# Optimization experiments

Hardware: AMD Instinct MI355X
Metric: run time of the kernel (lower is better)

The kernel has to match this reference:

```python
import jax, jax.numpy as jnp
import numpy as np
from jax import lax

INP_MODES = (4, 8, 8, 4)
OUT_MODES = (4, 8, 8, 4)
RANKS = (1, 8, 8, 8, 1)  # mat_ranks
WINDOW = (3, 3)


def setup_inputs() -> dict:
    key = jax.random.key(0)
    ks = jax.random.split(key, 7)
    d = {}
    d["x"] = jax.random.normal(ks[0], (16, 32, 32, 1024), jnp.float32)
    # conv filter: [kh, kw, 1, r0]
    d["filters"] = jax.random.normal(ks[1], (WINDOW[0], WINDOW[1], 1, RANKS[0]), jnp.float32) * (1.0 / 3.0)
    # TT cores: core_i has shape [m_i * r_{i+1}, r_i * n_i]
    for i in range(4):
        shp = (OUT_MODES[i] * RANKS[i + 1], RANKS[i] * INP_MODES[i])
        d[f"core{i}"] = jax.random.normal(ks[2 + i], shp, jnp.float32) * (1.0 / np.sqrt(shp[1]).astype(np.float32))
    d["bias"] = jnp.zeros((int(np.prod(OUT_MODES)),), jnp.float32)
    return d


def tt_conv(x, filters, cores, bias):
    B, H, W, C = x.shape  # C == prod(INP_MODES)
    r0 = filters.shape[3]
    # depthwise-style: every channel of every batch item becomes its own 1-channel map
    tmp = x.transpose(0, 3, 1, 2).reshape(B * C, H, W, 1)
    tmp = lax.conv_general_dilated(tmp, filters, window_strides=(1, 1), padding="SAME",
                                   dimension_numbers=("NHWC", "HWIO", "NHWC"))
    h, w = tmp.shape[1], tmp.shape[2]
    # [B, C, h, w, r0] -> [r0, C, B, h, w]
    tmp = tmp.reshape(B, C, h, w, r0).transpose(4, 1, 0, 2, 3)
    # chained TT-core contractions (fixed small loop over num_dim)
    for i in range(len(cores)):
        tmp = tmp.reshape(RANKS[i] * INP_MODES[i], -1)
        tmp = cores[i] @ tmp                      # [m_i * r_{i+1}, rest]
        tmp = tmp.reshape(OUT_MODES[i], -1).T     # move m_i to the back
    M = int(np.prod(OUT_MODES))
    out = tmp.reshape(-1, h, w, M) + bias
    return jax.nn.relu(out)


def reference(x, filters, core0, core1, core2, core3, bias):
    return tt_conv(x, filters, [core0, core1, core2, core3], bias)
```

## Files before the change

kernel.cpp:

```cpp
#include <hip/hip_runtime.h>
#include <hip/hip_bf16.h>
#include <stdint.h>

typedef __attribute__((ext_vector_type(8))) short short8;
typedef __attribute__((ext_vector_type(4))) float f32x4;

__device__ inline unsigned short f2bf(float f) {
  union { float f; unsigned u; } v; v.f = f;
  unsigned r = v.u + 0x7fffu + ((v.u >> 16) & 1u);
  return (unsigned short)(r >> 16);
}

__global__ __launch_bounds__(256) void tt_build_T(
    const float* __restrict__ c0, const float* __restrict__ c1,
    const float* __restrict__ c2, const float* __restrict__ c3,
    unsigned short* __restrict__ Tb) {
  __shared__ float L[8192];
  __shared__ float R[8192];
  int t = threadIdx.x;
  for (int i = t; i < 8192; i += 256) {
    int n1 = i & 7, n0 = (i >> 3) & 3, r2 = (i >> 5) & 7, m1 = (i >> 8) & 7, m0 = i >> 11;
    float s = 0.f;
#pragma unroll
    for (int r1 = 0; r1 < 8; ++r1)
      s += c0[(m0 * 8 + r1) * 4 + n0] * c1[(m1 * 8 + r2) * 64 + r1 * 8 + n1];
    L[i] = s;
  }
  for (int i = t; i < 8192; i += 256) {
    int n3 = i & 3, n2 = (i >> 2) & 7, m3 = (i >> 5) & 3, m2 = (i >> 7) & 7, r2 = i >> 10;
    float s = 0.f;
#pragma unroll
    for (int r3 = 0; r3 < 8; ++r3)
      s += c2[(m2 * 8 + r3) * 64 + r2 * 8 + n2] * c3[m3 * 32 + r3 * 4 + n3];
    R[i] = s;
  }
  __syncthreads();
  int base = blockIdx.x * 4096;
  for (int j = 0; j < 16; ++j) {
    int lin = j * 256 + t;
    int g = base + lin;
    int m = g >> 10, n = g & 1023;
    int m0 = m >> 8, m1 = (m >> 5) & 7, m2 = (m >> 2) & 7, m3 = m & 3;
    int n0 = n >> 8, n1 = (n >> 5) & 7, n2 = (n >> 2) & 7, n3 = n & 3;
    float s = 0.f;
#pragma unroll
    for (int r2 = 0; r2 < 8; ++r2)
      s += L[(((m0 * 8 + m1) * 8 + r2) * 4 + n0) * 8 + n1] *
           R[(((r2 * 8 + m2) * 4 + m3) * 8 + n2) * 4 + n3];
    Tb[(size_t)m * 1024 + n] = f2bf(s);
  }
}

__global__ __launch_bounds__(256) void tt_conv3x3_lds(
    const float* __restrict__ x, const float* __restrict__ filt,
    unsigned short* __restrict__ D) {
  __shared__ float xs[10][32][32];
  int bid = blockIdx.x;
  int cg = bid & 31, strip = (bid >> 5) & 3, b = bid >> 7;
  int h0 = strip * 8;
  int tid = threadIdx.x;
  float4 z4; z4.x = z4.y = z4.z = z4.w = 0.f;
#pragma unroll
  for (int i = 0; i < 10; ++i) {
    int j = tid + 256 * i;
    int row = j >> 8, w = (j >> 3) & 31, c4 = j & 7;
    int gh = h0 - 1 + row;
    float4 v = z4;
    if ((unsigned)gh < 32u)
      v = *reinterpret_cast<const float4*>(x + ((size_t)((b * 32 + gh) * 32 + w)) * 1024 + cg * 32 + c4 * 4);
    *reinterpret_cast<float4*>(&xs[row][w][c4 * 4]) = v;
  }
  float F[9];
#pragma unroll
  for (int i = 0; i < 9; ++i) F[i] = filt[i];
  __syncthreads();

  int c4 = tid & 7, w = tid >> 3;
#define LD3(r, d0, d1, d2) { \
    d1 = *reinterpret_cast<const float4*>(&xs[r][w][c4 * 4]); \
    d0 = (w > 0)  ? *reinterpret_cast<const float4*>(&xs[r][w - 1][c4 * 4]) : z4; \
    d2 = (w < 31) ? *reinterpret_cast<const float4*>(&xs[r][w + 1][c4 * 4]) : z4; }
#define ACC4(a, f, v) { a.x += (f) * v.x; a.y += (f) * v.y; a.z += (f) * v.z; a.w += (f) * v.w; }
  float4 a00, a01, a02, a10, a11, a12, a20, a21, a22;
  LD3(0, a00, a01, a02);
  LD3(1, a10, a11, a12);
#pragma unroll
  for (int h = 0; h < 8; ++h) {
    LD3(h + 2, a20, a21, a22);
    float4 s = z4;
    ACC4(s, F[0], a00); ACC4(s, F[1], a01); ACC4(s, F[2], a02);
    ACC4(s, F[3], a10); ACC4(s, F[4], a11); ACC4(s, F[5], a12);
    ACC4(s, F[6], a20); ACC4(s, F[7], a21); ACC4(s, F[8], a22);
    ushort4 o;
    o.x = f2bf(s.x); o.y = f2bf(s.y); o.z = f2bf(s.z); o.w = f2bf(s.w);
    *reinterpret_cast<ushort4*>(&D[((size_t)(b * 1024 + (h0 + h) * 32 + w)) * 1024 + cg * 32 + c4 * 4]) = o;
    a00 = a10; a01 = a11; a02 = a12;
    a10 = a20; a11 = a21; a12 = a22;
  }
#undef LD3
#undef ACC4
}

__device__ inline void stage16(const unsigned short* g, unsigned short* l) {
  __builtin_amdgcn_global_load_lds(
      (const __attribute__((address_space(1))) void*)g,
      (__attribute__((address_space(3))) void*)l, 16, 0, 0);
}

__global__ __launch_bounds__(512, 4) void tt_gemm_hi(
    const unsigned short* __restrict__ A,
    const unsigned short* __restrict__ Bt,
    const float* __restrict__ bias,
    float* __restrict__ C) {
  __shared__ unsigned short lds[3][12288];
  const int tid = threadIdx.x;
  const int lane = tid & 63, wave = tid >> 6;
  const int wr = wave >> 2, wc = wave & 3;
  const int lr = lane & 15, kc = lane >> 4;

  int bid = blockIdx.x;
  int swz = (bid & 7) * 64 + (bid >> 3);
  int brow = (swz & 127) * 128;
  int bcol = (swz >> 7) * 256;

  int rowA, cA, rowB0, cB0, rowB1, cB1;
  { int q = tid;       int li = q >> 3, sl = (q & 7) ^ (li & 7); rowA  = 2 * li + (sl >> 2); cA  = sl & 3; }
  { int q = tid;       int li = q >> 3, sl = (q & 7) ^ (li & 7); rowB0 = 2 * li + (sl >> 2); cB0 = sl & 3; }
  { int q = tid + 512; int li = q >> 3, sl = (q & 7) ^ (li & 7); rowB1 = 2 * li + (sl >> 2); cB1 = sl & 3; }
  const unsigned short* srcA  = A  + (size_t)(brow + rowA)  * 1024 + cA  * 8;
  const unsigned short* srcB0 = Bt + (size_t)(bcol + rowB0) * 1024 + cB0 * 8;
  const unsigned short* srcB1 = Bt + (size_t)(bcol + rowB1) * 1024 + cB1 * 8;
  const int la = tid * 8, lb0 = 4096 + tid * 8, lb1 = 8192 + tid * 8;

  int offA[4], offB[4];
#pragma unroll
  for (int m = 0; m < 4; ++m) {
    int row = wr * 64 + m * 16 + lr;
    int li = row >> 1, sl = (row & 1) * 4 + kc;
    offA[m] = (li * 8 + (sl ^ (li & 7))) * 8;
  }
#pragma unroll
  for (int n = 0; n < 4; ++n) {
    int row = wc * 64 + n * 16 + lr;
    int li = row >> 1, sl = (row & 1) * 4 + kc;
    offB[n] = 4096 + (li * 8 + (sl ^ (li & 7))) * 8;
  }

  f32x4 acc[4][4] = {};

#define STAGE(S, T) { \
    stage16(srcA  + (T) * 32, &lds[S][la]); \
    stage16(srcB0 + (T) * 32, &lds[S][lb0]); \
    stage16(srcB1 + (T) * 32, &lds[S][lb1]); }

#define KTILE(RB, SB, T2, VMS) { \
    if ((T2) >= 0) STAGE(SB, T2); \
    asm volatile("s_waitcnt vmcnt(" VMS ")" ::: "memory"); \
    __builtin_amdgcn_s_barrier(); \
    short8 af[4], bfr[4]; \
    _Pragma("unroll") for (int m = 0; m < 4; ++m) \
      af[m] = *reinterpret_cast<const short8*>(&lds[RB][offA[m]]); \
    _Pragma("unroll") for (int n = 0; n < 4; ++n) \
      bfr[n] = *reinterpret_cast<const short8*>(&lds[RB][offB[n]]); \
    _Pragma("unroll") for (int m = 0; m < 4; ++m) \
      _Pragma("unroll") for (int n = 0; n < 4; ++n) \
        acc[m][n] = __builtin_amdgcn_mfma_f32_16x16x32_bf16(bfr[n], af[m], acc[m][n], 0, 0, 0); \
    __builtin_amdgcn_s_barrier(); \
    __builtin_amdgcn_sched_barrier(0); }

  STAGE(0, 0);
  STAGE(1, 1);

  for (int t = 0; t < 30; t += 3) {
    KTILE(0, 2, t + 2, "6")
    KTILE(1, 0, t + 3, "6")
    KTILE(2, 1, t + 4, "6")
  }
  KTILE(0, 0, -1, "3")
  KTILE(1, 1, -1, "0")

#undef KTILE
#undef STAGE

#pragma unroll
  for (int n = 0; n < 4; ++n) {
    int col = bcol + wc * 64 + n * 16 + kc * 4;
    float4 bv = *reinterpret_cast<const float4*>(&bias[col]);
#pragma unroll
    for (int m = 0; m < 4; ++m) {
      int row = brow + wr * 64 + m * 16 + lr;
      f32x4 v = acc[m][n];
      float4 o;
      o.x = v[0] + bv.x; o.y = v[1] + bv.y; o.z = v[2] + bv.z; o.w = v[3] + bv.w;
      o.x = o.x > 0.f ? o.x : 0.f;
      o.y = o.y > 0.f ? o.y : 0.f;
      o.z = o.z > 0.f ? o.z : 0.f;
      o.w = o.w > 0.f ? o.w : 0.f;
      *reinterpret_cast<float4*>(&C[(size_t)row * 1024 + col]) = o;
    }
  }
}

extern "C" void kernel_launch(void* const* d_in, const int* in_sizes, int n_in,
                              void* d_out, int out_size, void* d_ws, size_t ws_size,
                              hipStream_t stream) {
  const float* x = (const float*)d_in[0];
  const float* filt = (const float*)d_in[1];
  const float* c0 = (const float*)d_in[2];
  const float* c1 = (const float*)d_in[3];
  const float* c2 = (const float*)d_in[4];
  const float* c3 = (const float*)d_in[5];
  const float* bias = (const float*)d_in[6];
  float* out = (float*)d_out;

  unsigned short* Tb = (unsigned short*)d_ws;
  unsigned short* D = Tb + (size_t)1024 * 1024;

  tt_build_T<<<256, 256, 0, stream>>>(c0, c1, c2, c3, Tb);
  tt_conv3x3_lds<<<2048, 256, 0, stream>>>(x, filt, D);
  tt_gemm_hi<<<512, 512, 0, stream>>>(D, Tb, bias, out);
}
```

Baseline: 86.07 us.

## Retile GEMM to 128x128 blocks with 4-stage LDS ring and one barrier

The bf16 MFMA GEMM changes from 512-thread blocks with 128x256 tiles to 256-thread blocks with 128x128 tiles, doubling the grid to 1024 blocks. The 3-buffer LDS pipeline becomes a 4-buffer ring. Each k-tile now has a single barrier, with the next prefetch issued right after it into the buffer read in the previous step, replacing the second barrier and sched_barrier. The aim is to cut synchronisation stalls and give better load balance across CUs. In exchange, B-tile reuse per block drops, and 64KB of LDS per block may limit how many blocks fit on a CU.

```diff
diff --git a/kernel.cpp b/kernel.cpp
--- a/kernel.cpp
+++ b/kernel.cpp
@@ -107,30 +107,31 @@
       (__attribute__((address_space(3))) void*)l, 16, 0, 0);
 }
 
-__global__ __launch_bounds__(512, 4) void tt_gemm_hi(
+__global__ __launch_bounds__(256, 4) void tt_gemm_r4(
     const unsigned short* __restrict__ A,
     const unsigned short* __restrict__ Bt,
     const float* __restrict__ bias,
     float* __restrict__ C) {
-  __shared__ unsigned short lds[3][12288];
+  __shared__ unsigned short lds[4][8192];
   const int tid = threadIdx.x;
   const int lane = tid & 63, wave = tid >> 6;
-  const int wr = wave >> 2, wc = wave & 3;
+  const int wr = wave >> 1, wc = wave & 1;
   const int lr = lane & 15, kc = lane >> 4;
 
   int bid = blockIdx.x;
-  int swz = (bid & 7) * 64 + (bid >> 3);
+  int swz = (bid & 7) * 128 + (bid >> 3);
   int brow = (swz & 127) * 128;
-  int bcol = (swz >> 7) * 256;
-
-  int rowA, cA, rowB0, cB0, rowB1, cB1;
-  { int q = tid;       int li = q >> 3, sl = (q & 7) ^ (li & 7); rowA  = 2 * li + (sl >> 2); cA  = sl & 3; }
-  { int q = tid;       int li = q >> 3, sl = (q & 7) ^ (li & 7); rowB0 = 2 * li + (sl >> 2); cB0 = sl & 3; }
-  { int q = tid + 512; int li = q >> 3, sl = (q & 7) ^ (li & 7); rowB1 = 2 * li + (sl >> 2); cB1 = sl & 3; }
-  const unsigned short* srcA  = A  + (size_t)(brow + rowA)  * 1024 + cA  * 8;
-  const unsigned short* srcB0 = Bt + (size_t)(bcol + rowB0) * 1024 + cB0 * 8;
-  const unsigned short* srcB1 = Bt + (size_t)(bcol + rowB1) * 1024 + cB1 * 8;
-  const int la = tid * 8, lb0 = 4096 + tid * 8, lb1 = 8192 + tid * 8;
+  int bcol = (swz >> 7) * 128;
+
+  int r0, c0x, r1, c1x;
+  { int q = tid;       int li = q >> 3, sl = (q & 7) ^ (li & 7); r0 = 2 * li + (sl >> 2); c0x = sl & 3; }
+  { int q = tid + 256; int li = q >> 3, sl = (q & 7) ^ (li & 7); r1 = 2 * li + (sl >> 2); c1x = sl & 3; }
+  const unsigned short* srcA0 = A  + (size_t)(brow + r0) * 1024 + c0x * 8;
+  const unsigned short* srcA1 = A  + (size_t)(brow + r1) * 1024 + c1x * 8;
+  const unsigned short* srcB0 = Bt + (size_t)(bcol + r0) * 1024 + c0x * 8;
+  const unsigned short* srcB1 = Bt + (size_t)(bcol + r1) * 1024 + c1x * 8;
+  const int la0 = tid * 8, la1 = (tid + 256) * 8;
+  const int lb0 = 4096 + tid * 8, lb1 = 4096 + (tid + 256) * 8;
 
   int offA[4], offB[4];
 #pragma unroll
@@ -149,14 +150,15 @@
   f32x4 acc[4][4] = {};
 
 #define STAGE(S, T) { \
-    stage16(srcA  + (T) * 32, &lds[S][la]); \
+    stage16(srcA0 + (T) * 32, &lds[S][la0]); \
+    stage16(srcA1 + (T) * 32, &lds[S][la1]); \
     stage16(srcB0 + (T) * 32, &lds[S][lb0]); \
     stage16(srcB1 + (T) * 32, &lds[S][lb1]); }
 
-#define KTILE(RB, SB, T2, VMS) { \
-    if ((T2) >= 0) STAGE(SB, T2); \
+#define KTILE(RB, T3, VMS) { \
     asm volatile("s_waitcnt vmcnt(" VMS ")" ::: "memory"); \
     __builtin_amdgcn_s_barrier(); \
+    if ((T3) >= 0) STAGE(((RB) + 3) & 3, T3); \
     short8 af[4], bfr[4]; \
     _Pragma("unroll") for (int m = 0; m < 4; ++m) \
       af[m] = *reinterpret_cast<const short8*>(&lds[RB][offA[m]]); \
@@ -164,20 +166,22 @@
       bfr[n] = *reinterpret_cast<const short8*>(&lds[RB][offB[n]]); \
     _Pragma("unroll") for (int m = 0; m < 4; ++m) \
       _Pragma("unroll") for (int n = 0; n < 4; ++n) \
-        acc[m][n] = __builtin_amdgcn_mfma_f32_16x16x32_bf16(bfr[n], af[m], acc[m][n], 0, 0, 0); \
-    __builtin_amdgcn_s_barrier(); \
-    __builtin_amdgcn_sched_barrier(0); }
+        acc[m][n] = __builtin_amdgcn_mfma_f32_16x16x32_bf16(bfr[n], af[m], acc[m][n], 0, 0, 0); }
 
   STAGE(0, 0);
   STAGE(1, 1);
-
-  for (int t = 0; t < 30; t += 3) {
-    KTILE(0, 2, t + 2, "6")
-    KTILE(1, 0, t + 3, "6")
-    KTILE(2, 1, t + 4, "6")
-  }
-  KTILE(0, 0, -1, "3")
-  KTILE(1, 1, -1, "0")
+  STAGE(2, 2);
+
+  for (int t = 0; t < 28; t += 4) {
+    KTILE(0, t + 3, "8")
+    KTILE(1, t + 4, "8")
+    KTILE(2, t + 5, "8")
+    KTILE(3, t + 6, "8")
+  }
+  KTILE(0, 31, "8")
+  KTILE(1, -1, "8")
+  KTILE(2, -1, "4")
+  KTILE(3, -1, "0")
 
 #undef KTILE
 #undef STAGE
@@ -218,5 +222,5 @@
 
   tt_build_T<<<256, 256, 0, stream>>>(c0, c1, c2, c3, Tb);
   tt_conv3x3_lds<<<2048, 256, 0, stream>>>(x, filt, D);
-  tt_gemm_hi<<<512, 512, 0, stream>>>(D, Tb, bias, out);
-}
+  tt_gemm_r4<<<1024, 256, 0, stream>>>(D, Tb, bias, out);
+}
```

Measured after the change: 98.69 us. 14.7% more time.

## Merge prep kernels and widen GEMM tile to 128x512 with split staging

Applied to the files above, without the earlier changes.

Folds the TT-matrix build and the 3x3 conv into one launch by dispatching on block index. The intermediate L/R factors are now held in bf16 to fit the shared LDS buffer. The GEMM tile widens from 128x256 to 128x512 per block, so each A tile is reused across more columns and only 256 blocks launch. Each k-step is split into two MFMA halves with staggered async loads and s_setprio around the MFMAs. The trade-offs are lower occupancy (2 blocks/SM, more LDS and accumulators), fewer blocks than CUs, and extra rounding in the T build.

```diff
diff --git a/kernel.cpp b/kernel.cpp
--- a/kernel.cpp
+++ b/kernel.cpp
@@ -10,55 +10,59 @@
   unsigned r = v.u + 0x7fffu + ((v.u >> 16) & 1u);
   return (unsigned short)(r >> 16);
 }
-
-__global__ __launch_bounds__(256) void tt_build_T(
+__device__ inline float bf2f(unsigned short u) {
+  union { unsigned u; float f; } v; v.u = ((unsigned)u) << 16; return v.f;
+}
+
+__global__ __launch_bounds__(256) void tt_prep(
+    const float* __restrict__ x, const float* __restrict__ filt,
     const float* __restrict__ c0, const float* __restrict__ c1,
     const float* __restrict__ c2, const float* __restrict__ c3,
-    unsigned short* __restrict__ Tb) {
-  __shared__ float L[8192];
-  __shared__ float R[8192];
-  int t = threadIdx.x;
-  for (int i = t; i < 8192; i += 256) {
-    int n1 = i & 7, n0 = (i >> 3) & 3, r2 = (i >> 5) & 7, m1 = (i >> 8) & 7, m0 = i >> 11;
-    float s = 0.f;
-#pragma unroll
-    for (int r1 = 0; r1 < 8; ++r1)
-      s += c0[(m0 * 8 + r1) * 4 + n0] * c1[(m1 * 8 + r2) * 64 + r1 * 8 + n1];
-    L[i] = s;
-  }
-  for (int i = t; i < 8192; i += 256) {
-    int n3 = i & 3, n2 = (i >> 2) & 7, m3 = (i >> 5) & 3, m2 = (i >> 7) & 7, r2 = i >> 10;
-    float s = 0.f;
-#pragma unroll
-    for (int r3 = 0; r3 < 8; ++r3)
-      s += c2[(m2 * 8 + r3) * 64 + r2 * 8 + n2] * c3[m3 * 32 + r3 * 4 + n3];
-    R[i] = s;
-  }
-  __syncthreads();
-  int base = blockIdx.x * 4096;
-  for (int j = 0; j < 16; ++j) {
-    int lin = j * 256 + t;
-    int g = base + lin;
-    int m = g >> 10, n = g & 1023;
-    int m0 = m >> 8, m1 = (m >> 5) & 7, m2 = (m >> 2) & 7, m3 = m & 3;
-    int n0 = n >> 8, n1 = (n >> 5) & 7, n2 = (n >> 2) & 7, n3 = n & 3;
-    float s = 0.f;
-#pragma unroll
-    for (int r2 = 0; r2 < 8; ++r2)
-      s += L[(((m0 * 8 + m1) * 8 + r2) * 4 + n0) * 8 + n1] *
-           R[(((r2 * 8 + m2) * 4 + m3) * 8 + n2) * 4 + n3];
-    Tb[(size_t)m * 1024 + n] = f2bf(s);
-  }
-}
-
-__global__ __launch_bounds__(256) void tt_conv3x3_lds(
-    const float* __restrict__ x, const float* __restrict__ filt,
-    unsigned short* __restrict__ D) {
-  __shared__ float xs[10][32][32];
-  int bid = blockIdx.x;
-  int cg = bid & 31, strip = (bid >> 5) & 3, b = bid >> 7;
+    unsigned short* __restrict__ Tb, unsigned short* __restrict__ D) {
+  __shared__ __align__(16) char smem[40960];
+  const int tid = threadIdx.x;
+  const int bid = blockIdx.x;
+
+  if (bid < 256) {
+    unsigned short* Lb = (unsigned short*)smem;
+    unsigned short* Rb = (unsigned short*)(smem + 16384);
+    for (int i = tid; i < 8192; i += 256) {
+      int n1 = i & 7, n0 = (i >> 3) & 3, r2 = (i >> 5) & 7, m1 = (i >> 8) & 7, m0 = i >> 11;
+      float s = 0.f;
+#pragma unroll
+      for (int r1 = 0; r1 < 8; ++r1)
+        s += c0[(m0 * 8 + r1) * 4 + n0] * c1[(m1 * 8 + r2) * 64 + r1 * 8 + n1];
+      Lb[i] = f2bf(s);
+    }
+    for (int i = tid; i < 8192; i += 256) {
+      int n3 = i & 3, n2 = (i >> 2) & 7, m3 = (i >> 5) & 3, m2 = (i >> 7) & 7, r2 = i >> 10;
+      float s = 0.f;
+#pragma unroll
+      for (int r3 = 0; r3 < 8; ++r3)
+        s += c2[(m2 * 8 + r3) * 64 + r2 * 8 + n2] * c3[m3 * 32 + r3 * 4 + n3];
+      Rb[i] = f2bf(s);
+    }
+    __syncthreads();
+    int base = bid * 4096;
+    for (int j = 0; j < 16; ++j) {
+      int g = base + j * 256 + tid;
+      int m = g >> 10, n = g & 1023;
+      int m0 = m >> 8, m1 = (m >> 5) & 7, m2 = (m >> 2) & 7, m3 = m & 3;
+      int n0 = n >> 8, n1 = (n >> 5) & 7, n2 = (n >> 2) & 7, n3 = n & 3;
+      float s = 0.f;
+#pragma unroll
+      for (int r2 = 0; r2 < 8; ++r2)
+        s += bf2f(Lb[(((m0 * 8 + m1) * 8 + r2) * 4 + n0) * 8 + n1]) *
+             bf2f(Rb[(((r2 * 8 + m2) * 4 + m3) * 8 + n2) * 4 + n3]);
+      Tb[(size_t)m * 1024 + n] = f2bf(s);
+    }
+    return;
+  }
+
+  float (*xs)[32][32] = (float(*)[32][32])smem;
+  int cb = bid - 256;
+  int cg = cb & 31, strip = (cb >> 5) & 3, b = cb >> 7;
   int h0 = strip * 8;
-  int tid = threadIdx.x;
   float4 z4; z4.x = z4.y = z4.z = z4.w = 0.f;
 #pragma unroll
   for (int i = 0; i < 10; ++i) {
@@ -107,32 +111,38 @@
       (__attribute__((address_space(3))) void*)l, 16, 0, 0);
 }
 
-__global__ __launch_bounds__(512, 4) void tt_gemm_hi(
+__global__ __launch_bounds__(512, 2) void tt_gemm_n5(
     const unsigned short* __restrict__ A,
     const unsigned short* __restrict__ Bt,
     const float* __restrict__ bias,
     float* __restrict__ C) {
-  __shared__ unsigned short lds[3][12288];
+  __shared__ unsigned short lds[3][20480];
   const int tid = threadIdx.x;
   const int lane = tid & 63, wave = tid >> 6;
   const int wr = wave >> 2, wc = wave & 3;
   const int lr = lane & 15, kc = lane >> 4;
 
   int bid = blockIdx.x;
-  int swz = (bid & 7) * 64 + (bid >> 3);
-  int brow = (swz & 127) * 128;
-  int bcol = (swz >> 7) * 256;
-
-  int rowA, cA, rowB0, cB0, rowB1, cB1;
-  { int q = tid;       int li = q >> 3, sl = (q & 7) ^ (li & 7); rowA  = 2 * li + (sl >> 2); cA  = sl & 3; }
-  { int q = tid;       int li = q >> 3, sl = (q & 7) ^ (li & 7); rowB0 = 2 * li + (sl >> 2); cB0 = sl & 3; }
-  { int q = tid + 512; int li = q >> 3, sl = (q & 7) ^ (li & 7); rowB1 = 2 * li + (sl >> 2); cB1 = sl & 3; }
-  const unsigned short* srcA  = A  + (size_t)(brow + rowA)  * 1024 + cA  * 8;
-  const unsigned short* srcB0 = Bt + (size_t)(bcol + rowB0) * 1024 + cB0 * 8;
-  const unsigned short* srcB1 = Bt + (size_t)(bcol + rowB1) * 1024 + cB1 * 8;
-  const int la = tid * 8, lb0 = 4096 + tid * 8, lb1 = 8192 + tid * 8;
-
-  int offA[4], offB[4];
+  int panel = (bid & 7) >> 2;
+  int mtile = ((bid >> 3) << 2) | (bid & 3);
+  int brow = mtile * 128, bcol = panel * 512;
+
+  int rowA, kA;
+  { int q = tid; int li = q >> 3, sl = (q & 7) ^ (li & 7); rowA = 2 * li + (sl >> 2); kA = (sl & 3) * 8; }
+  const unsigned short* srcA = A + (size_t)(brow + rowA) * 1024 + kA;
+  const int la = tid * 8;
+  const unsigned short* srcB[4];
+  int lb[4];
+#pragma unroll
+  for (int j = 0; j < 4; ++j) {
+    int q = tid + 512 * j;
+    int li = q >> 3, sl = (q & 7) ^ (li & 7);
+    int row = 2 * li + (sl >> 2), k = (sl & 3) * 8;
+    srcB[j] = Bt + (size_t)(bcol + row) * 1024 + k;
+    lb[j] = 4096 + q * 8;
+  }
+
+  int offA[4], offB[8];
 #pragma unroll
   for (int m = 0; m < 4; ++m) {
     int row = wr * 64 + m * 16 + lr;
@@ -140,51 +150,68 @@
     offA[m] = (li * 8 + (sl ^ (li & 7))) * 8;
   }
 #pragma unroll
-  for (int n = 0; n < 4; ++n) {
-    int row = wc * 64 + n * 16 + lr;
+  for (int n = 0; n < 8; ++n) {
+    int row = wc * 128 + n * 16 + lr;
     int li = row >> 1, sl = (row & 1) * 4 + kc;
     offB[n] = 4096 + (li * 8 + (sl ^ (li & 7))) * 8;
   }
 
-  f32x4 acc[4][4] = {};
-
-#define STAGE(S, T) { \
-    stage16(srcA  + (T) * 32, &lds[S][la]); \
-    stage16(srcB0 + (T) * 32, &lds[S][lb0]); \
-    stage16(srcB1 + (T) * 32, &lds[S][lb1]); }
+  f32x4 acc[4][8] = {};
+
+#define STAGE_B01(S, T) { stage16(srcB[0] + (T) * 32, &lds[S][lb[0]]); \
+                          stage16(srcB[1] + (T) * 32, &lds[S][lb[1]]); }
+#define STAGE_AB23(S, T) { stage16(srcA + (T) * 32, &lds[S][la]); \
+                           stage16(srcB[2] + (T) * 32, &lds[S][lb[2]]); \
+                           stage16(srcB[3] + (T) * 32, &lds[S][lb[3]]); }
 
 #define KTILE(RB, SB, T2, VMS) { \
-    if ((T2) >= 0) STAGE(SB, T2); \
+    short8 af[4]; \
+    if ((T2) >= 0) STAGE_B01(SB, T2); \
     asm volatile("s_waitcnt vmcnt(" VMS ")" ::: "memory"); \
     __builtin_amdgcn_s_barrier(); \
-    short8 af[4], bfr[4]; \
-    _Pragma("unroll") for (int m = 0; m < 4; ++m) \
-      af[m] = *reinterpret_cast<const short8*>(&lds[RB][offA[m]]); \
-    _Pragma("unroll") for (int n = 0; n < 4; ++n) \
-      bfr[n] = *reinterpret_cast<const short8*>(&lds[RB][offB[n]]); \
-    _Pragma("unroll") for (int m = 0; m < 4; ++m) \
+    { short8 bf0[4]; \
+      _Pragma("unroll") for (int m = 0; m < 4; ++m) \
+        af[m] = *reinterpret_cast<const short8*>(&lds[RB][offA[m]]); \
       _Pragma("unroll") for (int n = 0; n < 4; ++n) \
-        acc[m][n] = __builtin_amdgcn_mfma_f32_16x16x32_bf16(bfr[n], af[m], acc[m][n], 0, 0, 0); \
+        bf0[n] = *reinterpret_cast<const short8*>(&lds[RB][offB[n]]); \
+      asm volatile("s_waitcnt lgkmcnt(0)"); \
+      __builtin_amdgcn_s_setprio(1); \
+      _Pragma("unroll") for (int m = 0; m < 4; ++m) \
+        _Pragma("unroll") for (int n = 0; n < 4; ++n) \
+          acc[m][n] = __builtin_amdgcn_mfma_f32_16x16x32_bf16(bf0[n], af[m], acc[m][n], 0, 0, 0); \
+      __builtin_amdgcn_s_setprio(0); } \
     __builtin_amdgcn_s_barrier(); \
-    __builtin_amdgcn_sched_barrier(0); }
-
-  STAGE(0, 0);
-  STAGE(1, 1);
+    if ((T2) >= 0) STAGE_AB23(SB, T2); \
+    __builtin_amdgcn_s_barrier(); \
+    { short8 bf1[4]; \
+      _Pragma("unroll") for (int n = 0; n < 4; ++n) \
+        bf1[n] = *reinterpret_cast<const short8*>(&lds[RB][offB[4 + n]]); \
+      asm volatile("s_waitcnt lgkmcnt(0)"); \
+      __builtin_amdgcn_s_setprio(1); \
+      _Pragma("unroll") for (int m = 0; m < 4; ++m) \
+        _Pragma("unroll") for (int n = 0; n < 4; ++n) \
+          acc[m][4 + n] = __builtin_amdgcn_mfma_f32_16x16x32_bf16(bf1[n], af[m], acc[m][4 + n], 0, 0, 0); \
+      __builtin_amdgcn_s_setprio(0); } \
+    __builtin_amdgcn_s_barrier(); }
+
+  STAGE_B01(0, 0); STAGE_AB23(0, 0);
+  STAGE_B01(1, 1); STAGE_AB23(1, 1);
 
   for (int t = 0; t < 30; t += 3) {
-    KTILE(0, 2, t + 2, "6")
-    KTILE(1, 0, t + 3, "6")
-    KTILE(2, 1, t + 4, "6")
-  }
-  KTILE(0, 0, -1, "3")
+    KTILE(0, 2, t + 2, "7")
+    KTILE(1, 0, t + 3, "7")
+    KTILE(2, 1, t + 4, "7")
+  }
+  KTILE(0, 0, -1, "5")
   KTILE(1, 1, -1, "0")
 
 #undef KTILE
-#undef STAGE
-
-#pragma unroll
-  for (int n = 0; n < 4; ++n) {
-    int col = bcol + wc * 64 + n * 16 + kc * 4;
+#undef STAGE_B01
+#undef STAGE_AB23
+
+#pragma unroll
+  for (int n = 0; n < 8; ++n) {
+    int col = bcol + wc * 128 + n * 16 + kc * 4;
     float4 bv = *reinterpret_cast<const float4*>(&bias[col]);
 #pragma unroll
     for (int m = 0; m < 4; ++m) {
@@ -216,7 +243,6 @@
   unsigned short* Tb = (unsigned short*)d_ws;
   unsigned short* D = Tb + (size_t)1024 * 1024;
 
-  tt_build_T<<<256, 256, 0, stream>>>(c0, c1, c2, c3, Tb);
-  tt_conv3x3_lds<<<2048, 256, 0, stream>>>(x, filt, D);
-  tt_gemm_hi<<<512, 512, 0, stream>>>(D, Tb, bias, out);
-}
+  tt_prep<<<2304, 256, 0, stream>>>(x, filt, c0, c1, c2, c3, Tb, D);
+  tt_gemm_n5<<<256, 512, 0, stream>>>(D, Tb, bias, out);
+}
```

New measurement: 74.81 us. 1.15x faster.
